# Kernel tuning notes

Measured on AMD Instinct MI355X. Metric: run time of the kernel, lower is better.

Reference implementation:

```python
import jax, jax.numpy as jnp
import numpy as np

N = 100000   # nodes
E = 3200000  # edges
HIGH, LOW, EMB, HID, OUT = 384, 64, 128, 128, 2

def setup_inputs() -> dict:
    key = jax.random.key(0)
    ks = jax.random.split(key, 12)
    def lin(k, fan_in, fan_out):
        bound = 1.0 / np.sqrt(fan_in)
        kw, kb = jax.random.split(k)
        W = jax.random.uniform(kw, (fan_in, fan_out), jnp.float32, -bound, bound)
        b = jax.random.uniform(kb, (fan_out,), jnp.float32, -bound, bound)
        return W, b
    W_emb, b_emb = lin(ks[0], LOW, EMB)
    W1, b1 = lin(ks[1], HIGH + EMB, HID)
    W2, b2 = lin(ks[2], HID, HID)
    W_lin, b_lin = lin(ks[3], HID, OUT)
    return {
        "high_dim_features": jax.random.normal(ks[4], (N, HIGH), jnp.float32),
        "low_dim_features": jax.random.normal(ks[5], (N, LOW), jnp.float32),
        "edge_index": jax.random.randint(ks[6], (2, E), 0, N, jnp.int32),
        "W_emb": W_emb, "b_emb": b_emb,
        "W1": W1, "b1": b1,
        "W2": W2, "b2": b2,
        "W_lin": W_lin, "b_lin": b_lin,
    }

def _gcn_conv(x, W, b, src, dst, dis):
    # GCNConv: add self-loops, symmetric normalization D^-1/2 (A+I) D^-1/2
    xl = x @ W                                   # [N, out]
    norm = dis[src] * dis[dst]                   # [E]
    agg = jax.ops.segment_sum(xl[src] * norm[:, None], dst, num_segments=N)
    agg = agg + xl * (dis * dis)[:, None]        # self-loop term
    return agg + b

def reference(high_dim_features, low_dim_features, edge_index,
              W_emb, b_emb, W1, b1, W2, b2, W_lin, b_lin):
    src, dst = edge_index[0], edge_index[1]
    # degree with self-loops, computed on destination nodes (PyG default)
    deg = jax.ops.segment_sum(jnp.ones((E,), jnp.float32), dst, num_segments=N) + 1.0
    dis = jax.lax.rsqrt(deg)                     # deg >= 1 always

    low_emb = jax.nn.relu(low_dim_features @ W_emb + b_emb)
    x = jnp.concatenate([high_dim_features, low_emb], axis=1)  # [N, HIGH+EMB]
    x = jax.nn.relu(_gcn_conv(x, W1, b1, src, dst, dis))
    # dropout is identity in eval mode
    x = jax.nn.relu(_gcn_conv(x, W2, b2, src, dst, dis))
    x = x @ W_lin + b_lin
    return jax.nn.log_softmax(x, axis=1)
```

## Files before the change

kernel.cpp:

```cpp
#include <hip/hip_runtime.h>

#define HIGH 384
#define LOWD 64
#define EMB  128
#define HID  128

#define BINSHIFT 8
#define SRCBITS  17
#define SRCMASK  0x1FFFF
#define NBLK     256

typedef unsigned int u32;
typedef unsigned short u16;
typedef unsigned char u8;
typedef __attribute__((ext_vector_type(8))) short bf16x8;
typedef __attribute__((ext_vector_type(4))) float f32x4;
typedef __attribute__((ext_vector_type(2))) float f32x2;

__device__ __forceinline__ u32 pack_bf16(float a, float b) {
    u32 ua = __builtin_bit_cast(u32, a);
    u32 ub = __builtin_bit_cast(u32, b);
    ua += 0x7fffu + ((ua >> 16) & 1u);
    ub += 0x7fffu + ((ub >> 16) & 1u);
    return (ua >> 16) | (ub & 0xffff0000u);
}
__device__ __forceinline__ u16 pack1_bf16(float a) {
    u32 ua = __builtin_bit_cast(u32, a);
    ua += 0x7fffu + ((ua >> 16) & 1u);
    return (u16)(ua >> 16);
}
__device__ __forceinline__ u8 pack1_fp8(float a) {
    int r = __builtin_amdgcn_cvt_pk_fp8_f32(a, a, 0, false);
    return (u8)(r & 0xff);
}


__global__ void k_castw_all(const float* __restrict__ W1, u16* __restrict__ Wt1,
                            const float* __restrict__ W2, u16* __restrict__ Wt2,
                            const float* __restrict__ WE, u16* __restrict__ WtE) {
    int i = blockIdx.x * 256 + threadIdx.x;
    if (i < 65536) {
        int k = i >> 7, c = i & 127;
        Wt1[c * 512 + k] = pack1_bf16(W1[i]);
    } else if (i < 81920) {
        int j = i - 65536;
        int k = j >> 7, c = j & 127;
        Wt2[c * 128 + k] = pack1_bf16(W2[j]);
    } else if (i < 90112) {
        int j = i - 81920;
        int k = j >> 7, c = j & 127;
        WtE[c * 64 + k] = pack1_bf16(WE[j]);
    }
}


__global__ __launch_bounds__(256) void k_binhist(const int* __restrict__ dst, int E,
                                                 int* __restrict__ cnts, int NB) {
    __shared__ int hist[512];
    for (int b = threadIdx.x; b < NB; b += 256) hist[b] = 0;
    __syncthreads();
    int CH = (E + gridDim.x - 1) / gridDim.x;
    int e0 = blockIdx.x * CH;
    int e1 = min(E, e0 + CH);
    for (int e = e0 + threadIdx.x; e < e1; e += 256)
        atomicAdd(&hist[dst[e] >> BINSHIFT], 1);
    __syncthreads();
    for (int b = threadIdx.x; b < NB; b += 256)
        cnts[b * NBLK + blockIdx.x] = hist[b];
}

__global__ __launch_bounds__(256) void k_binscatter(const int* __restrict__ src,
                                                    const int* __restrict__ dst, int E,
                                                    const int* __restrict__ cnts,
                                                    u32* __restrict__ packed, int NB) {
    __shared__ int cur[512];
    for (int b = threadIdx.x; b < NB; b += 256) cur[b] = cnts[b * NBLK + blockIdx.x];
    __syncthreads();
    int CH = (E + gridDim.x - 1) / gridDim.x;
    int e0 = blockIdx.x * CH;
    int e1 = min(E, e0 + CH);
    for (int e = e0 + threadIdx.x; e < e1; e += 256) {
        int d = dst[e];
        int s = src[e];
        int bin = d >> BINSHIFT;
        int pos = atomicAdd(&cur[bin], 1);
        packed[pos] = (u32)s | ((u32)(d & 255) << SRCBITS);
    }
}

__global__ __launch_bounds__(256) void k_csrbin(
    const u32* __restrict__ packed, const int* __restrict__ cnts, int E,
    int* __restrict__ row_start, float* __restrict__ dis,
    int* __restrict__ csr, int NB, int N)
{
    __shared__ int hist[256];
    __shared__ int sc[256];
    int t = threadIdx.x;
    int b = blockIdx.x;
    int begin = cnts[b * NBLK];
    int end = (b + 1 < NB) ? cnts[(b + 1) * NBLK] : E;

    hist[t] = 0;
    __syncthreads();
    for (int e = begin + t; e < end; e += 256)
        atomicAdd(&hist[packed[e] >> SRCBITS], 1);
    __syncthreads();
    int deg = hist[t];

    sc[t] = deg;
    __syncthreads();
    int x = deg;
    for (int off = 1; off < 256; off <<= 1) {
        int y = (t >= off) ? sc[t - off] : 0;
        __syncthreads();
        x += y; sc[t] = x;
        __syncthreads();
    }
    int rs = begin + (x - deg);

    int node = (b << BINSHIFT) + t;
    if (node < N) {
        row_start[node] = rs;
        dis[node] = rsqrtf((float)deg + 1.0f);
    }
    if (b == NB - 1 && t == 0) row_start[N] = E;

    hist[t] = rs;
    __syncthreads();
    for (int e = begin + t; e < end; e += 256) {
        u32 p = packed[e];
        int pos = atomicAdd(&hist[p >> SRCBITS], 1);
        csr[pos] = (int)((p & SRCMASK) << 5);
    }
}


__global__ void k_scan1(const int* __restrict__ in, int n, int* __restrict__ bsums) {
    __shared__ int sh[256];
    int t = threadIdx.x;
    int base = blockIdx.x * 1024 + t * 4;
    int s = 0;
#pragma unroll
    for (int j = 0; j < 4; j++) { int idx = base + j; s += (idx < n) ? in[idx] : 0; }
    sh[t] = s; __syncthreads();
    for (int off = 128; off > 0; off >>= 1) {
        if (t < off) sh[t] += sh[t + off];
        __syncthreads();
    }
    if (t == 0) bsums[blockIdx.x] = sh[0];
}

__global__ void k_scan2(int* bsums, int nb) {
    if (threadIdx.x == 0 && blockIdx.x == 0) {
        int run = 0;
        for (int i = 0; i < nb; i++) { int v = bsums[i]; bsums[i] = run; run += v; }
    }
}

__global__ void k_scan3_flat(int* __restrict__ data, int n, const int* __restrict__ bsums) {
    __shared__ int sh[256];
    int t = threadIdx.x;
    int base = blockIdx.x * 1024 + t * 4;
    int v[4]; int s = 0;
#pragma unroll
    for (int j = 0; j < 4; j++) { int idx = base + j; v[j] = (idx < n) ? data[idx] : 0; s += v[j]; }
    sh[t] = s; __syncthreads();
    int x = s;
    for (int off = 1; off < 256; off <<= 1) {
        int y = (t >= off) ? sh[t - off] : 0;
        __syncthreads();
        x += y; sh[t] = x;
        __syncthreads();
    }
    int run = bsums[blockIdx.x] + (x - s);
#pragma unroll
    for (int j = 0; j < 4; j++) {
        int idx = base + j;
        if (idx < n) data[idx] = run;
        run += v[j];
    }
}


template<bool A1BF, bool BIAS, bool RELU, bool SCALE, int OUT>
__global__ __launch_bounds__(256, 6) void k_mgemm(
    const void* __restrict__ A1v, int K1,
    const u32* __restrict__ A2, int K2,
    const u16* __restrict__ Wt,
    const float* __restrict__ bias,
    const float* __restrict__ dis,
    void* __restrict__ Cv, int M)
{
    __shared__ u32 Als[2][64][16];
    __shared__ u32 Bls[2][128][16];

    const int tid = threadIdx.x;
    const int l = tid & 63;
    const int w = tid >> 6;
    const int g = l >> 4;
    const int lr = l & 15;
    const int blockRow = blockIdx.x * 64;
    const int K = K1 + K2;
    const int T = K >> 5;

    const int ar = tid >> 2;
    const int ak = tid & 3;
    int arow = blockRow + ar; if (arow >= M) arow = M - 1;
    const int awb = (ak + ((ar >> 1) & 3)) & 3;

    const int wc = tid >> 1;
    const int wh = tid & 1;
    const int wsw = (wc >> 1) & 3;
    const int wb0 = (wh * 2 + wsw) & 3;
    const int wb1 = (wh * 2 + 1 + wsw) & 3;

    const float* a1f = (const float*)A1v + (size_t)arow * K1;
    const u32*   a1b = (const u32*)A1v + (size_t)arow * (K1 >> 1);
    const u32*   a2b = A2 + (size_t)arow * (K2 >> 1);
    const u32*   wtb = (const u32*)Wt + (size_t)wc * (K >> 1);

    f32x4 acc[8];
#pragma unroll
    for (int j = 0; j < 8; j++) acc[j] = (f32x4)0.f;

    u32 pa0[4], wk0[8], pa1[4], wk1[8];

    auto load_tile = [&](int k0, u32* pa, u32* wk) {
        if (k0 < K1) {
            if (A1BF) {
                uint4 a = *(const uint4*)(a1b + (k0 >> 1) + ak * 4);
                pa[0] = a.x; pa[1] = a.y; pa[2] = a.z; pa[3] = a.w;
            } else {
                const float* src = a1f + k0 + ak * 8;
                float4 f0 = *(const float4*)(src + 0);
                float4 f1 = *(const float4*)(src + 4);
                pa[0] = pack_bf16(f0.x, f0.y); pa[1] = pack_bf16(f0.z, f0.w);
                pa[2] = pack_bf16(f1.x, f1.y); pa[3] = pack_bf16(f1.z, f1.w);
            }
        } else {
            uint4 a = *(const uint4*)(a2b + ((k0 - K1) >> 1) + ak * 4);
            pa[0] = a.x; pa[1] = a.y; pa[2] = a.z; pa[3] = a.w;
        }
        const u32* srcw = wtb + ((k0 + wh * 16) >> 1);
        uint4 a = *(const uint4*)srcw;
        uint4 b = *(const uint4*)(srcw + 4);
        wk[0] = a.x; wk[1] = a.y; wk[2] = a.z; wk[3] = a.w;
        wk[4] = b.x; wk[5] = b.y; wk[6] = b.z; wk[7] = b.w;
    };
    auto store_tile = [&](int buf, const u32* pa, const u32* wk) {
        *(uint4*)&Als[buf][ar][awb * 4] = make_uint4(pa[0], pa[1], pa[2], pa[3]);
        *(uint4*)&Bls[buf][wc][wb0 * 4] = make_uint4(wk[0], wk[1], wk[2], wk[3]);
        *(uint4*)&Bls[buf][wc][wb1 * 4] = make_uint4(wk[4], wk[5], wk[6], wk[7]);
    };
    auto compute = [&](int cur) {
        bf16x8 af;
        {
            int r = w * 16 + lr;
            int blk = (g + ((r >> 1) & 3)) & 3;
            af = *(const bf16x8*)&Als[cur][r][blk * 4];
        }
#pragma unroll
        for (int cb = 0; cb < 8; cb++) {
            int c = cb * 16 + lr;
            int blk = (g + ((c >> 1) & 3)) & 3;
            bf16x8 bf = *(const bf16x8*)&Bls[cur][c][blk * 4];
            acc[cb] = __builtin_amdgcn_mfma_f32_16x16x32_bf16(af, bf, acc[cb], 0, 0, 0);
        }
    };

    load_tile(0, pa0, wk0);
    load_tile(32, pa1, wk1);
    store_tile(0, pa0, wk0);
    __syncthreads();

    for (int t = 0; t < T; t += 2) {
        if (t + 2 < T) load_tile((t + 2) << 5, pa0, wk0);
        compute(0);
        store_tile(1, pa1, wk1);
        __syncthreads();
        if (t + 3 < T) load_tile((t + 3) << 5, pa1, wk1);
        compute(1);
        if (t + 2 < T) store_tile(0, pa0, wk0);
        __syncthreads();
    }

    float disv[4];
    if (SCALE) {
#pragma unroll
        for (int j = 0; j < 4; j++) {
            int row = blockRow + w * 16 + g * 4 + j;
            disv[j] = (row < M) ? dis[row] : 0.f;
        }
    }
#pragma unroll
    for (int cb = 0; cb < 8; cb++) {
        int col = cb * 16 + lr;
        float bv = BIAS ? bias[col] : 0.f;
#pragma unroll
        for (int j = 0; j < 4; j++) {
            int row = blockRow + w * 16 + g * 4 + j;
            if (row < M) {
                float v = acc[cb][j];
                if (BIAS) v += bv;
                if (SCALE) v *= disv[j];
                if (RELU) v = fmaxf(v, 0.f);
                if (OUT == 0) {
                    ((u16*)Cv)[(size_t)row * 128 + col] = pack1_bf16(v);
                } else {
                    ((u8*)Cv)[(size_t)row * 128 + col] = pack1_fp8(v);
                }
            }
        }
    }
}


template<int MODE>
__global__ __launch_bounds__(256) void k_gatherw(
    const u32* __restrict__ xls32, const int* __restrict__ row_start,
    const int* __restrict__ csr, const float* __restrict__ dis,
    const float* __restrict__ bias, const float* __restrict__ Wl,
    const float* __restrict__ bl, void* __restrict__ outv, int N)
{
    int wave = threadIdx.x >> 6;
    int lane = threadIdx.x & 63;
    int half = lane >> 5;
    int w32 = lane & 31;
    int n = blockIdx.x * 4 + wave;
    if (n >= N) return;
    int jb = row_start[n], je = row_start[n + 1];

    float a0 = 0.f, a1 = 0.f, a2 = 0.f, a3 = 0.f;
    {
        u32 v = xls32[(u32)n * 32 + w32];
        if (half == 0) {
            f32x2 lo = __builtin_amdgcn_cvt_pk_f32_fp8((int)v, false);
            f32x2 hi = __builtin_amdgcn_cvt_pk_f32_fp8((int)v, true);
            a0 = lo.x; a1 = lo.y; a2 = hi.x; a3 = hi.y;
        }
    }

    int j = jb;
    for (; j + 7 < je; j += 8) {
        int c0 = csr[j + 4 * half + 0];
        int c1 = csr[j + 4 * half + 1];
        int c2 = csr[j + 4 * half + 2];
        int c3 = csr[j + 4 * half + 3];
        u32 v0 = xls32[(u32)c0 + w32];
        u32 v1 = xls32[(u32)c1 + w32];
        u32 v2 = xls32[(u32)c2 + w32];
        u32 v3 = xls32[(u32)c3 + w32];
        f32x2 l0 = __builtin_amdgcn_cvt_pk_f32_fp8((int)v0, false);
        f32x2 h0 = __builtin_amdgcn_cvt_pk_f32_fp8((int)v0, true);
        f32x2 l1 = __builtin_amdgcn_cvt_pk_f32_fp8((int)v1, false);
        f32x2 h1 = __builtin_amdgcn_cvt_pk_f32_fp8((int)v1, true);
        f32x2 l2 = __builtin_amdgcn_cvt_pk_f32_fp8((int)v2, false);
        f32x2 h2 = __builtin_amdgcn_cvt_pk_f32_fp8((int)v2, true);
        f32x2 l3 = __builtin_amdgcn_cvt_pk_f32_fp8((int)v3, false);
        f32x2 h3 = __builtin_amdgcn_cvt_pk_f32_fp8((int)v3, true);
        a0 += (l0.x + l1.x) + (l2.x + l3.x);
        a1 += (l0.y + l1.y) + (l2.y + l3.y);
        a2 += (h0.x + h1.x) + (h2.x + h3.x);
        a3 += (h0.y + h1.y) + (h2.y + h3.y);
    }
    for (; j + 3 < je; j += 4) {
        int c0 = csr[j + 2 * half];
        int c1 = csr[j + 2 * half + 1];
        u32 v0 = xls32[(u32)c0 + w32];
        u32 v1 = xls32[(u32)c1 + w32];
        f32x2 l0 = __builtin_amdgcn_cvt_pk_f32_fp8((int)v0, false);
        f32x2 h0 = __builtin_amdgcn_cvt_pk_f32_fp8((int)v0, true);
        f32x2 l1 = __builtin_amdgcn_cvt_pk_f32_fp8((int)v1, false);
        f32x2 h1 = __builtin_amdgcn_cvt_pk_f32_fp8((int)v1, true);
        a0 += l0.x + l1.x; a1 += l0.y + l1.y;
        a2 += h0.x + h1.x; a3 += h0.y + h1.y;
    }
    if (j + 1 < je) {
        int c = csr[j + half];
        u32 v = xls32[(u32)c + w32];
        f32x2 lo = __builtin_amdgcn_cvt_pk_f32_fp8((int)v, false);
        f32x2 hi = __builtin_amdgcn_cvt_pk_f32_fp8((int)v, true);
        a0 += lo.x; a1 += lo.y; a2 += hi.x; a3 += hi.y;
        j += 2;
    }
    if (j < je) {
        int c = csr[j];
        u32 v = xls32[(u32)c + w32];
        if (half == 0) {
            f32x2 lo = __builtin_amdgcn_cvt_pk_f32_fp8((int)v, false);
            f32x2 hi = __builtin_amdgcn_cvt_pk_f32_fp8((int)v, true);
            a0 += lo.x; a1 += lo.y; a2 += hi.x; a3 += hi.y;
        }
    }

    a0 += __shfl(a0, w32 + 32);
    a1 += __shfl(a1, w32 + 32);
    a2 += __shfl(a2, w32 + 32);
    a3 += __shfl(a3, w32 + 32);

    float d = dis[n];
    float4 bv = *(const float4*)&bias[w32 * 4];
    float h0v = fmaxf(fmaf(d, a0, bv.x), 0.f);
    float h1v = fmaxf(fmaf(d, a1, bv.y), 0.f);
    float h2v = fmaxf(fmaf(d, a2, bv.z), 0.f);
    float h3v = fmaxf(fmaf(d, a3, bv.w), 0.f);

    if (MODE == 0) {
        if (half == 0) {
            uint2 pw;
            pw.x = pack_bf16(h0v, h1v);
            pw.y = pack_bf16(h2v, h3v);
            *(uint2*)((u32*)outv + (size_t)n * 64 + w32 * 2) = pw;
        }
    } else {
        float4 q0 = *(const float4*)&Wl[w32 * 8];
        float4 q1 = *(const float4*)&Wl[w32 * 8 + 4];
        float p0 = h0v * q0.x + h1v * q0.z + h2v * q1.x + h3v * q1.z;
        float p1 = h0v * q0.y + h1v * q0.w + h2v * q1.y + h3v * q1.w;
#pragma unroll
        for (int off = 16; off > 0; off >>= 1) {
            p0 += __shfl_down(p0, off);
            p1 += __shfl_down(p1, off);
        }
        if (lane == 0) {
            float z0 = p0 + bl[0], z1 = p1 + bl[1];
            float m = fmaxf(z0, z1);
            float ls = m + logf(expf(z0 - m) + expf(z1 - m));
            float* out = (float*)outv;
            out[(size_t)n * 2 + 0] = z0 - ls;
            out[(size_t)n * 2 + 1] = z1 - ls;
        }
    }
}


extern "C" void kernel_launch(void* const* d_in, const int* in_sizes, int n_in,
                              void* d_out, int out_size, void* d_ws, size_t ws_size,
                              hipStream_t stream) {
    const float* high  = (const float*)d_in[0];
    const float* low   = (const float*)d_in[1];
    const int*   ei    = (const int*)d_in[2];
    const float* W_emb = (const float*)d_in[3];
    const float* b_emb = (const float*)d_in[4];
    const float* W1    = (const float*)d_in[5];
    const float* b1    = (const float*)d_in[6];
    const float* W2    = (const float*)d_in[7];
    const float* b2    = (const float*)d_in[8];
    const float* Wl    = (const float*)d_in[9];
    const float* bl    = (const float*)d_in[10];

    int N = in_sizes[0] / HIGH;
    int E = in_sizes[2] / 2;
    const int* srcp = ei;
    const int* dstp = ei + E;
    float* out = (float*)d_out;

    int NB = (N + 255) >> BINSHIFT;
    int NSCAN = NB * NBLK;

    char* ws = (char*)d_ws;
    size_t off = 0;
    auto alloc = [&](size_t b) { size_t o = off; off += (b + 255) & ~(size_t)255; return o; };
    float* dis       = (float*)(ws + alloc((size_t)N * 4));
    int*   row_start = (int*)  (ws + alloc((size_t)(N + 1) * 4));
    int*   bsums     = (int*)  (ws + alloc(4096));
    int*   cnts      = (int*)  (ws + alloc((size_t)NSCAN * 4));
    u32*   packed    = (u32*)  (ws + alloc((size_t)E * 4));
    int*   csr       = (int*)  (ws + alloc((size_t)E * 4));
    u16*   Wt1       = (u16*)  (ws + alloc((size_t)512 * 128 * 2));
    u16*   Wt2       = (u16*)  (ws + alloc((size_t)128 * 128 * 2));
    u16*   WtE       = (u16*)  (ws + alloc((size_t)64 * 128 * 2));
    u16*   bufE      = (u16*)  (ws + alloc((size_t)N * 128 * 2));
    u8*    bufX      = (u8*)   (ws + alloc((size_t)N * 128));
    u16*   bufH      = (u16*)  (ws + alloc((size_t)N * 128 * 2));
    (void)ws_size; (void)n_in; (void)out_size;

    int nbS = (NSCAN + 1023) / 1024;
    int mt  = (N + 63) / 64;

    k_castw_all<<<(90112 + 255) / 256, 256, 0, stream>>>(W1, Wt1, W2, Wt2, W_emb, WtE);

    k_binhist<<<NBLK, 256, 0, stream>>>(dstp, E, cnts, NB);
    k_scan1<<<nbS, 256, 0, stream>>>(cnts, NSCAN, bsums);
    k_scan2<<<1, 64, 0, stream>>>(bsums, nbS);
    k_scan3_flat<<<nbS, 256, 0, stream>>>(cnts, NSCAN, bsums);
    k_binscatter<<<NBLK, 256, 0, stream>>>(srcp, dstp, E, cnts, packed, NB);
    k_csrbin<<<NB, 256, 0, stream>>>(packed, cnts, E, row_start, dis, csr, NB, N);

    k_mgemm<false, true, true, false, 0><<<mt, 256, 0, stream>>>(
        low, LOWD, (const u32*)bufE, 0, WtE, b_emb, nullptr, bufE, N);
    k_mgemm<false, false, false, true, 1><<<mt, 256, 0, stream>>>(
        high, HIGH, (const u32*)bufE, EMB, Wt1, nullptr, dis, bufX, N);
    k_gatherw<0><<<(N + 3) / 4, 256, 0, stream>>>(
        (const u32*)bufX, row_start, csr, dis, b1, nullptr, nullptr, bufH, N);
    k_mgemm<true, false, false, true, 1><<<mt, 256, 0, stream>>>(
        bufH, HID, (const u32*)bufH, 0, Wt2, nullptr, dis, bufX, N);
    k_gatherw<1><<<(N + 3) / 4, 256, 0, stream>>>(
        (const u32*)bufX, row_start, csr, dis, b2, Wl, bl, out, N);
}
```

Baseline: 369.9 us.

## Replace tiled GEMM with persistent kernel keeping full weight matrix in LDS

The double-buffered LDS-tiled GEMM is replaced with a persistent kernel of 256 blocks × 768 threads. Each block loads the whole transposed weight matrix into XOR-swizzled shared memory once. Each wave then processes 32-row tiles, loading A fragments straight from global memory into registers with no LDS staging and no per-step barriers. The aim is to cut weight reloads and synchronisation. The cost is a large LDS footprint (128 KB for K=512), one block per CU, and latency hiding that now depends only on register double-buffering.

Result: slower. 625.4 us (+69.1%).

```diff
diff --git a/kernel.cpp b/kernel.cpp
--- a/kernel.cpp
+++ b/kernel.cpp
@@ -182,132 +182,139 @@
 }
 
 
-template<bool A1BF, bool BIAS, bool RELU, bool SCALE, int OUT>
-__global__ __launch_bounds__(256, 6) void k_mgemm(
-    const void* __restrict__ A1v, int K1,
-    const u32* __restrict__ A2, int K2,
+template<int K1, int K2, bool A1BF, bool BIAS, bool RELU, bool SCALE, int OUT>
+__global__ __launch_bounds__(768, 1) void k_pgemm(
+    const void* __restrict__ A1v,
+    const u16* __restrict__ A2h,
     const u16* __restrict__ Wt,
     const float* __restrict__ bias,
     const float* __restrict__ dis,
-    void* __restrict__ Cv, int M)
+    void* __restrict__ Cv, int M, int ntiles)
 {
-    __shared__ u32 Als[2][64][16];
-    __shared__ u32 Bls[2][128][16];
+    constexpr int K = K1 + K2;
+    constexpr int T = K >> 5;
+    constexpr int KCH = K >> 3;
+    static_assert((T & 1) == 0, "T must be even");
+    __shared__ __align__(16) u32 Wl[128 * (K >> 1)];
 
     const int tid = threadIdx.x;
+
+    for (int i = tid; i < 128 * KCH; i += 768) {
+        int c = i / KCH, ch = i % KCH;
+        int phys = ch ^ (c & 7);
+        uint4 v = *(const uint4*)(Wt + (size_t)c * K + ch * 8);
+        *(uint4*)&Wl[c * (K >> 1) + phys * 4] = v;
+    }
+    __syncthreads();
+
     const int l = tid & 63;
     const int w = tid >> 6;
     const int g = l >> 4;
     const int lr = l & 15;
-    const int blockRow = blockIdx.x * 64;
-    const int K = K1 + K2;
-    const int T = K >> 5;
-
-    const int ar = tid >> 2;
-    const int ak = tid & 3;
-    int arow = blockRow + ar; if (arow >= M) arow = M - 1;
-    const int awb = (ak + ((ar >> 1) & 3)) & 3;
-
-    const int wc = tid >> 1;
-    const int wh = tid & 1;
-    const int wsw = (wc >> 1) & 3;
-    const int wb0 = (wh * 2 + wsw) & 3;
-    const int wb1 = (wh * 2 + 1 + wsw) & 3;
-
-    const float* a1f = (const float*)A1v + (size_t)arow * K1;
-    const u32*   a1b = (const u32*)A1v + (size_t)arow * (K1 >> 1);
-    const u32*   a2b = A2 + (size_t)arow * (K2 >> 1);
-    const u32*   wtb = (const u32*)Wt + (size_t)wc * (K >> 1);
-
-    f32x4 acc[8];
-#pragma unroll
-    for (int j = 0; j < 8; j++) acc[j] = (f32x4)0.f;
-
-    u32 pa0[4], wk0[8], pa1[4], wk1[8];
-
-    auto load_tile = [&](int k0, u32* pa, u32* wk) {
-        if (k0 < K1) {
-            if (A1BF) {
-                uint4 a = *(const uint4*)(a1b + (k0 >> 1) + ak * 4);
-                pa[0] = a.x; pa[1] = a.y; pa[2] = a.z; pa[3] = a.w;
+
+    for (int t = blockIdx.x * 12 + w; t < ntiles; t += gridDim.x * 12) {
+        const int r0 = t * 32;
+        int rlo = r0 + lr;       if (rlo >= M) rlo = M - 1;
+        int rhi = r0 + 16 + lr;  if (rhi >= M) rhi = M - 1;
+
+        const float* a1fl = (const float*)A1v + (size_t)rlo * K1 + g * 8;
+        const float* a1fh = (const float*)A1v + (size_t)rhi * K1 + g * 8;
+        const u16*   a1hl = (const u16*)A1v + (size_t)rlo * K1 + g * 8;
+        const u16*   a1hh = (const u16*)A1v + (size_t)rhi * K1 + g * 8;
+        const u16*   a2hl = A2h + (size_t)rlo * K2 + g * 8;
+        const u16*   a2hh = A2h + (size_t)rhi * K2 + g * 8;
+
+        f32x4 acc[2][8];
+#pragma unroll
+        for (int a = 0; a < 2; a++)
+#pragma unroll
+            for (int j = 0; j < 8; j++) acc[a][j] = (f32x4)0.f;
+
+        u32 pkA[8], pkB[8];
+
+        auto load_pk = [&](int i, u32* pk) {
+            const int k0 = i * 32;
+            if (K2 == 0 || k0 < K1) {
+                if (A1BF) {
+                    uint4 a = *(const uint4*)(a1hl + k0);
+                    uint4 b = *(const uint4*)(a1hh + k0);
+                    pk[0] = a.x; pk[1] = a.y; pk[2] = a.z; pk[3] = a.w;
+                    pk[4] = b.x; pk[5] = b.y; pk[6] = b.z; pk[7] = b.w;
+                } else {
+                    const float* sl = a1fl + k0;
+                    const float* sh2 = a1fh + k0;
+                    float4 f0 = *(const float4*)(sl);
+                    float4 f1 = *(const float4*)(sl + 4);
+                    float4 f2 = *(const float4*)(sh2);
+                    float4 f3 = *(const float4*)(sh2 + 4);
+                    pk[0] = pack_bf16(f0.x, f0.y); pk[1] = pack_bf16(f0.z, f0.w);
+                    pk[2] = pack_bf16(f1.x, f1.y); pk[3] = pack_bf16(f1.z, f1.w);
+                    pk[4] = pack_bf16(f2.x, f2.y); pk[5] = pack_bf16(f2.z, f2.w);
+                    pk[6] = pack_bf16(f3.x, f3.y); pk[7] = pack_bf16(f3.z, f3.w);
+                }
             } else {
-                const float* src = a1f + k0 + ak * 8;
-                float4 f0 = *(const float4*)(src + 0);
-                float4 f1 = *(const float4*)(src + 4);
-                pa[0] = pack_bf16(f0.x, f0.y); pa[1] = pack_bf16(f0.z, f0.w);
-                pa[2] = pack_bf16(f1.x, f1.y); pa[3] = pack_bf16(f1.z, f1.w);
+                uint4 a = *(const uint4*)(a2hl + (k0 - K1));
+                uint4 b = *(const uint4*)(a2hh + (k0 - K1));
+                pk[0] = a.x; pk[1] = a.y; pk[2] = a.z; pk[3] = a.w;
+                pk[4] = b.x; pk[5] = b.y; pk[6] = b.z; pk[7] = b.w;
             }
-        } else {
-            uint4 a = *(const uint4*)(a2b + ((k0 - K1) >> 1) + ak * 4);
-            pa[0] = a.x; pa[1] = a.y; pa[2] = a.z; pa[3] = a.w;
-        }
-        const u32* srcw = wtb + ((k0 + wh * 16) >> 1);
-        uint4 a = *(const uint4*)srcw;
-        uint4 b = *(const uint4*)(srcw + 4);
-        wk[0] = a.x; wk[1] = a.y; wk[2] = a.z; wk[3] = a.w;
-        wk[4] = b.x; wk[5] = b.y; wk[6] = b.z; wk[7] = b.w;
-    };
-    auto store_tile = [&](int buf, const u32* pa, const u32* wk) {
-        *(uint4*)&Als[buf][ar][awb * 4] = make_uint4(pa[0], pa[1], pa[2], pa[3]);
-        *(uint4*)&Bls[buf][wc][wb0 * 4] = make_uint4(wk[0], wk[1], wk[2], wk[3]);
-        *(uint4*)&Bls[buf][wc][wb1 * 4] = make_uint4(wk[4], wk[5], wk[6], wk[7]);
-    };
-    auto compute = [&](int cur) {
-        bf16x8 af;
-        {
-            int r = w * 16 + lr;
-            int blk = (g + ((r >> 1) & 3)) & 3;
-            af = *(const bf16x8*)&Als[cur][r][blk * 4];
-        }
-#pragma unroll
-        for (int cb = 0; cb < 8; cb++) {
-            int c = cb * 16 + lr;
-            int blk = (g + ((c >> 1) & 3)) & 3;
-            bf16x8 bf = *(const bf16x8*)&Bls[cur][c][blk * 4];
-            acc[cb] = __builtin_amdgcn_mfma_f32_16x16x32_bf16(af, bf, acc[cb], 0, 0, 0);
-        }
-    };
-
-    load_tile(0, pa0, wk0);
-    load_tile(32, pa1, wk1);
-    store_tile(0, pa0, wk0);
-    __syncthreads();
-
-    for (int t = 0; t < T; t += 2) {
-        if (t + 2 < T) load_tile((t + 2) << 5, pa0, wk0);
-        compute(0);
-        store_tile(1, pa1, wk1);
-        __syncthreads();
-        if (t + 3 < T) load_tile((t + 3) << 5, pa1, wk1);
-        compute(1);
-        if (t + 2 < T) store_tile(0, pa0, wk0);
-        __syncthreads();
-    }
-
-    float disv[4];
-    if (SCALE) {
-#pragma unroll
-        for (int j = 0; j < 4; j++) {
-            int row = blockRow + w * 16 + g * 4 + j;
-            disv[j] = (row < M) ? dis[row] : 0.f;
-        }
-    }
-#pragma unroll
-    for (int cb = 0; cb < 8; cb++) {
-        int col = cb * 16 + lr;
-        float bv = BIAS ? bias[col] : 0.f;
-#pragma unroll
-        for (int j = 0; j < 4; j++) {
-            int row = blockRow + w * 16 + g * 4 + j;
-            if (row < M) {
-                float v = acc[cb][j];
-                if (BIAS) v += bv;
-                if (SCALE) v *= disv[j];
-                if (RELU) v = fmaxf(v, 0.f);
-                if (OUT == 0) {
-                    ((u16*)Cv)[(size_t)row * 128 + col] = pack1_bf16(v);
-                } else {
-                    ((u8*)Cv)[(size_t)row * 128 + col] = pack1_fp8(v);
+        };
+
+        auto compute = [&](int i, const u32* pk) {
+            uint4 qa = make_uint4(pk[0], pk[1], pk[2], pk[3]);
+            uint4 qb = make_uint4(pk[4], pk[5], pk[6], pk[7]);
+            bf16x8 af0 = __builtin_bit_cast(bf16x8, qa);
+            bf16x8 af1 = __builtin_bit_cast(bf16x8, qb);
+            const int chb = i * 4 + g;
+#pragma unroll
+            for (int cb = 0; cb < 8; cb++) {
+                int c = cb * 16 + lr;
+                int phys = chb ^ (c & 7);
+                bf16x8 bf = *(const bf16x8*)&Wl[c * (K >> 1) + phys * 4];
+                acc[0][cb] = __builtin_amdgcn_mfma_f32_16x16x32_bf16(af0, bf, acc[0][cb], 0, 0, 0);
+                acc[1][cb] = __builtin_amdgcn_mfma_f32_16x16x32_bf16(af1, bf, acc[1][cb], 0, 0, 0);
+            }
+        };
+
+        load_pk(0, pkA);
+#pragma unroll
+        for (int i = 0; i < T; i += 2) {
+            if (i + 1 < T) load_pk(i + 1, pkB);
+            compute(i, pkA);
+            if (i + 2 < T) load_pk(i + 2, pkA);
+            compute(i + 1, pkB);
+        }
+
+        float disv[2][4];
+        if (SCALE) {
+#pragma unroll
+            for (int rf = 0; rf < 2; rf++)
+#pragma unroll
+                for (int j = 0; j < 4; j++) {
+                    int row = r0 + rf * 16 + g * 4 + j;
+                    disv[rf][j] = (row < M) ? dis[row] : 0.f;
+                }
+        }
+#pragma unroll
+        for (int rf = 0; rf < 2; rf++) {
+#pragma unroll
+            for (int cb = 0; cb < 8; cb++) {
+                int col = cb * 16 + lr;
+                float bv = BIAS ? bias[col] : 0.f;
+#pragma unroll
+                for (int j = 0; j < 4; j++) {
+                    int row = r0 + rf * 16 + g * 4 + j;
+                    if (row < M) {
+                        float v = acc[rf][cb][j];
+                        if (BIAS) v += bv;
+                        if (SCALE) v *= disv[rf][j];
+                        if (RELU) v = fmaxf(v, 0.f);
+                        if (OUT == 0) {
+                            ((u16*)Cv)[(size_t)row * 128 + col] = pack1_bf16(v);
+                        } else {
+                            ((u8*)Cv)[(size_t)row * 128 + col] = pack1_fp8(v);
+                        }
+                    }
                 }
             }
         }
@@ -476,7 +483,7 @@
     (void)ws_size; (void)n_in; (void)out_size;
 
     int nbS = (NSCAN + 1023) / 1024;
-    int mt  = (N + 63) / 64;
+    int ntiles = (N + 31) / 32;
 
     k_castw_all<<<(90112 + 255) / 256, 256, 0, stream>>>(W1, Wt1, W2, Wt2, W_emb, WtE);
 
@@ -487,14 +494,14 @@
     k_binscatter<<<NBLK, 256, 0, stream>>>(srcp, dstp, E, cnts, packed, NB);
     k_csrbin<<<NB, 256, 0, stream>>>(packed, cnts, E, row_start, dis, csr, NB, N);
 
-    k_mgemm<false, true, true, false, 0><<<mt, 256, 0, stream>>>(
-        low, LOWD, (const u32*)bufE, 0, WtE, b_emb, nullptr, bufE, N);
-    k_mgemm<false, false, false, true, 1><<<mt, 256, 0, stream>>>(
-        high, HIGH, (const u32*)bufE, EMB, Wt1, nullptr, dis, bufX, N);
+    k_pgemm<LOWD, 0, false, true, true, false, 0><<<256, 768, 0, stream>>>(
+        low, nullptr, WtE, b_emb, nullptr, bufE, N, ntiles);
+    k_pgemm<HIGH, EMB, false, false, false, true, 1><<<256, 768, 0, stream>>>(
+        high, bufE, Wt1, nullptr, dis, bufX, N, ntiles);
     k_gatherw<0><<<(N + 3) / 4, 256, 0, stream>>>(
         (const u32*)bufX, row_start, csr, dis, b1, nullptr, nullptr, bufH, N);
-    k_mgemm<true, false, false, true, 1><<<mt, 256, 0, stream>>>(
-        bufH, HID, (const u32*)bufH, 0, Wt2, nullptr, dis, bufX, N);
+    k_pgemm<HID, 0, true, false, false, true, 1><<<256, 768, 0, stream>>>(
+        bufH, nullptr, Wt2, nullptr, dis, bufX, N, ntiles);
     k_gatherw<1><<<(N + 3) / 4, 256, 0, stream>>>(
         (const u32*)bufX, row_start, csr, dis, b2, Wl, bl, out, N);
 }
```
